# Performance work log

Hardware: AMD Instinct MI355X
Metric: run time of the kernel (lower is better)

The kernel has to match this reference:

```python
import jax, jax.numpy as jnp
import numpy as np

EPS = 1e-5
C = 1.0
SQRT_C = 1.0
MAX_NORM = 0.95


def _log0(y):
    # log map at origin: atanh(sqrt(c)||y||) * y / (sqrt(c)||y||)
    norm = jnp.clip(jnp.linalg.norm(y, axis=-1, keepdims=True), EPS)
    arg = jnp.clip(SQRT_C * norm, None, 1.0 - EPS)
    return jnp.arctanh(arg) * y / (SQRT_C * norm)


def _exp0(v):
    # exp map at origin: tanh(sqrt(c)||v||) * v / (sqrt(c)||v||)
    norm = jnp.clip(jnp.linalg.norm(v, axis=-1, keepdims=True), EPS)
    return jnp.tanh(SQRT_C * norm) * v / (SQRT_C * norm)


def _proj(x):
    # project onto Poincare ball of radius MAX_NORM/sqrt(c)
    max_r = MAX_NORM / SQRT_C
    norm = jnp.linalg.norm(x, axis=-1, keepdims=True)
    return jnp.where(norm > max_r, x * max_r / jnp.clip(norm, EPS), x)


def _hyp_linear(x, W, b):
    # log -> euclidean linear -> exp -> project
    v = _log0(x)
    v = v @ W.T + b
    return _proj(_exp0(v))


def _hyp_graph_conv(x, src, dst, n_nodes, Wm, bm, Wu, bu):
    # 1. hyperbolic linear message transform
    h = _hyp_linear(x, Wm, bm)
    # 2. tangent-space (hyperbolic) mean aggregation over incoming edges
    t = _log0(h[src])                                   # [E, D]
    summed = jax.ops.segment_sum(t, dst, num_segments=n_nodes)
    cnt = jax.ops.segment_sum(jnp.ones((src.shape[0], 1), t.dtype), dst,
                              num_segments=n_nodes)
    agg = _proj(_exp0(summed / jnp.clip(cnt, 1.0)))
    # 3. hyperbolic linear update
    return _hyp_linear(agg, Wu, bu)


def setup_inputs() -> dict:
    key = jax.random.key(0)
    k1, k2, k3, k4 = jax.random.split(key, 4)
    N, E, D, L = 50000, 800000, 128, 2
    x = jax.random.normal(k1, (N, D), dtype=jnp.float32) * 0.01
    edge_index = jax.random.randint(k2, (2, E), 0, N, dtype=jnp.int32)
    msg_W = jax.random.normal(k3, (L, D, D), dtype=jnp.float32) * 0.05
    msg_b = jnp.zeros((L, D), dtype=jnp.float32)
    upd_W = jax.random.normal(k4, (L, D, D), dtype=jnp.float32) * 0.05
    upd_b = jnp.zeros((L, D), dtype=jnp.float32)
    return {"x": x, "edge_index": edge_index, "msg_W": msg_W, "msg_b": msg_b,
            "upd_W": upd_W, "upd_b": upd_b}


def reference(x, edge_index, msg_W, msg_b, upd_W, upd_b):
    src, dst = edge_index[0], edge_index[1]
    n_nodes = x.shape[0]
    h = x
    for l in range(msg_W.shape[0]):  # small fixed layer count
        h = _hyp_graph_conv(h, src, dst, n_nodes,
                            msg_W[l], msg_b[l], upd_W[l], upd_b[l])
    return h
```

## Files before the change

### kernel.cpp

```cpp
#include <hip/hip_runtime.h>
#include <math.h>

#define EPSF 1e-5f
#define MAXN 0.95f
#define DD 128

typedef unsigned short u16;
typedef __attribute__((ext_vector_type(8))) __bf16 bf16x8;
typedef __attribute__((ext_vector_type(4))) float f32x4;
typedef __attribute__((ext_vector_type(8))) unsigned short u16x8;
typedef __attribute__((ext_vector_type(4))) unsigned u32x4;

#define MFMA16 __builtin_amdgcn_mfma_f32_16x16x32_bf16

__device__ __forceinline__ u16 f2bf(float f) {
    unsigned u = __float_as_uint(f);
    return (u16)((u + 0x7FFFu + ((u >> 16) & 1u)) >> 16);
}
__device__ __forceinline__ float bf2f(u16 b) {
    return __uint_as_float(((unsigned)b) << 16);
}

__device__ __forceinline__ float chain_scale(float nrm, bool log_out) {
    float nc  = fmaxf(nrm, EPSF);
    float f   = tanhf(nc) / nc;
    float wn  = f * nrm;
    float p   = (wn > MAXN) ? (MAXN / fmaxf(wn, EPSF)) : 1.f;
    float s   = f * p;
    if (log_out) {
        float n2  = wn * p;
        float n2c = fmaxf(n2, EPSF);
        float arg = fminf(n2c, 1.f - EPSF);
        s *= atanhf(arg) / n2c;
    }
    return s;
}

__device__ __forceinline__ float agg_scale(const float* __restrict__ ssum,
                                           const int* __restrict__ rowptr,
                                           int rg) {
    int cnt = max(rowptr[rg + 1] - rowptr[rg], 1);
    float inv = 1.f / (float)cnt;
    return chain_scale(sqrtf(ssum[rg]) * inv, true) * inv;
}

__global__ __launch_bounds__(256)
void zero_int4(int4* __restrict__ p, int n4)
{
    int i = blockIdx.x * 256 + threadIdx.x;
    if (i < n4) p[i] = make_int4(0, 0, 0, 0);
}

__global__ __launch_bounds__(256)
void split_w(const float* __restrict__ msgW, const float* __restrict__ updW,
             u16* __restrict__ whi, u16* __restrict__ wlo, int L)
{
    int gid = blockIdx.x * 256 + threadIdx.x;
    int total = L * 2 * DD * DD;
    if (gid >= total) return;
    int mat = gid >> 14;
    int elem = gid & (DD * DD - 1);
    int l = mat >> 1, tpe = mat & 1;
    float f = (tpe ? updW : msgW)[(size_t)l * DD * DD + elem];
    u16 hb = f2bf(f);
    whi[gid] = hb;
    wlo[gid] = f2bf(f - bf2f(hb));
}

template<int LOG_OUT, int FP32_OUT, int F32_IN, int SCALE_IN>
__global__ __launch_bounds__(256)
void mfma_linear(const u16* __restrict__ vhi, const float* __restrict__ xin,
                 const float* __restrict__ ssum, const int* __restrict__ rowptr,
                 const u16* __restrict__ whi, const u16* __restrict__ wlo,
                 const float* __restrict__ bias,
                 u16* __restrict__ ohi, float* __restrict__ ofp, int N)
{
    __shared__ float sred[4][32];
    __shared__ float sScale[32];
    __shared__ float sSin[SCALE_IN ? 32 : 1];
    __shared__ u16 sHi[FP32_OUT ? 1 : 32][136];

    const int tid  = threadIdx.x;
    const int w    = tid >> 6;
    const int lane = tid & 63;
    const int l15  = lane & 15, lk = lane >> 4;
    const int base = blockIdx.x * 32;

    if (SCALE_IN) {
        if (tid < 32) {
            int rg = base + tid;
            sSin[tid] = agg_scale(ssum, rowptr, rg < N ? rg : (N - 1));
        }
        __syncthreads();
    }

    bf16x8 wh[2][4], wl[2][4];
    #pragma unroll
    for (int nt = 0; nt < 2; ++nt) {
        const int j = w * 32 + nt * 16 + l15;
        #pragma unroll
        for (int kt = 0; kt < 4; ++kt) {
            const int off = j * DD + kt * 32 + lk * 8;
            wh[nt][kt] = *(const bf16x8*)(whi + off);
            wl[nt][kt] = *(const bf16x8*)(wlo + off);
        }
    }
    const float bv0 = bias[w * 32 + l15];
    const float bv1 = bias[w * 32 + 16 + l15];

    f32x4 acc[2][2];
    #pragma unroll
    for (int mt = 0; mt < 2; ++mt)
        #pragma unroll
        for (int nt = 0; nt < 2; ++nt)
            acc[mt][nt] = (f32x4){0.f, 0.f, 0.f, 0.f};

    #pragma unroll
    for (int mt = 0; mt < 2; ++mt) {
        int row = base + mt * 16 + l15;
        row = (row < N) ? row : (N - 1);
        bf16x8 ah[4];
        if (F32_IN) {
            const float* xr = xin + (size_t)row * DD + lk * 8;
            float fv[32];
            float ss = 0.f;
            #pragma unroll
            for (int kt = 0; kt < 4; ++kt) {
                float4 a = *(const float4*)(xr + kt * 32);
                float4 b = *(const float4*)(xr + kt * 32 + 4);
                fv[kt*8+0]=a.x; fv[kt*8+1]=a.y; fv[kt*8+2]=a.z; fv[kt*8+3]=a.w;
                fv[kt*8+4]=b.x; fv[kt*8+5]=b.y; fv[kt*8+6]=b.z; fv[kt*8+7]=b.w;
            }
            #pragma unroll
            for (int q = 0; q < 32; ++q) ss += fv[q] * fv[q];
            ss += __shfl_xor(ss, 16);
            ss += __shfl_xor(ss, 32);
            float nc = fmaxf(sqrtf(ss), EPSF);
            float sc = atanhf(fminf(nc, 1.f - EPSF)) / nc;
            #pragma unroll
            for (int kt = 0; kt < 4; ++kt) {
                u16x8 uh;
                #pragma unroll
                for (int q = 0; q < 8; ++q)
                    uh[q] = f2bf(fv[kt*8+q] * sc);
                ah[kt] = *reinterpret_cast<bf16x8*>(&uh);
            }
        } else {
            const size_t ro = (size_t)row * DD + lk * 8;
            #pragma unroll
            for (int kt = 0; kt < 4; ++kt)
                ah[kt] = *(const bf16x8*)(vhi + ro + kt * 32);
        }
        #pragma unroll
        for (int kt = 0; kt < 4; ++kt) {
            #pragma unroll
            for (int nt = 0; nt < 2; ++nt) {
                acc[mt][nt] = MFMA16(ah[kt], wh[nt][kt], acc[mt][nt], 0, 0, 0);
                acc[mt][nt] = MFMA16(ah[kt], wl[nt][kt], acc[mt][nt], 0, 0, 0);
            }
        }
    }

    #pragma unroll
    for (int mt = 0; mt < 2; ++mt) {
        #pragma unroll
        for (int r = 0; r < 4; ++r) {
            const float sv = SCALE_IN ? sSin[mt*16 + lk*4 + r] : 1.f;
            float y0 = acc[mt][0][r] * sv + bv0;
            float y1 = acc[mt][1][r] * sv + bv1;
            float part = y0 * y0 + y1 * y1;
            part += __shfl_xor(part, 1);
            part += __shfl_xor(part, 2);
            part += __shfl_xor(part, 4);
            part += __shfl_xor(part, 8);
            if (l15 == 0) sred[w][mt*16 + lk*4 + r] = part;
        }
    }
    __syncthreads();
    if (tid < 32) {
        float ss = sred[0][tid] + sred[1][tid] + sred[2][tid] + sred[3][tid];
        sScale[tid] = chain_scale(sqrtf(ss), LOG_OUT != 0);
    }
    __syncthreads();

    #pragma unroll
    for (int mt = 0; mt < 2; ++mt) {
        #pragma unroll
        for (int r = 0; r < 4; ++r) {
            const int rloc = mt*16 + lk*4 + r;
            const float s = sScale[rloc];
            const float sv = SCALE_IN ? sSin[rloc] : 1.f;
            #pragma unroll
            for (int nt = 0; nt < 2; ++nt) {
                float z = (acc[mt][nt][r] * sv + (nt ? bv1 : bv0)) * s;
                const int col = w*32 + nt*16 + l15;
                if (FP32_OUT) {
                    const int rg = base + rloc;
                    if (rg < N) ofp[(size_t)rg * DD + col] = z;
                } else {
                    sHi[rloc][col] = f2bf(z);
                }
            }
        }
    }
    if (!FP32_OUT) {
        __syncthreads();
        const int row = tid >> 3, qc = (tid & 7) * 16;
        const int rg = base + row;
        if (rg < N) {
            #pragma unroll
            for (int i = 0; i < 2; ++i)
                *(u16x8*)(ohi + (size_t)rg * DD + qc + i*8) =
                    *(const u16x8*)(&sHi[row][qc + i*8]);
        }
    }
}

__global__ __launch_bounds__(256)
void mfma_linear_fused(const u16* __restrict__ vhi,
                       const float* __restrict__ ssum, const int* __restrict__ rowptr,
                       const u16* __restrict__ wuh, const u16* __restrict__ wul,
                       const float* __restrict__ bu,
                       const u16* __restrict__ wmh, const u16* __restrict__ wml,
                       const float* __restrict__ bm,
                       u16* __restrict__ ohi, int N)
{
    __shared__ float sred[4][32];
    __shared__ float sScale[32];
    __shared__ float sSin[32];
    __shared__ u16 sHi[32][136];

    const int tid  = threadIdx.x;
    const int w    = tid >> 6;
    const int lane = tid & 63;
    const int l15  = lane & 15, lk = lane >> 4;
    const int base = blockIdx.x * 32;

    if (tid < 32) {
        int rg = base + tid;
        sSin[tid] = agg_scale(ssum, rowptr, rg < N ? rg : (N - 1));
    }
    __syncthreads();

    f32x4 acc[2][2];

    {
        bf16x8 wh[2][4], wl[2][4];
        #pragma unroll
        for (int nt = 0; nt < 2; ++nt) {
            const int j = w * 32 + nt * 16 + l15;
            #pragma unroll
            for (int kt = 0; kt < 4; ++kt) {
                const int off = j * DD + kt * 32 + lk * 8;
                wh[nt][kt] = *(const bf16x8*)(wuh + off);
                wl[nt][kt] = *(const bf16x8*)(wul + off);
            }
        }
        const float bv0 = bu[w * 32 + l15];
        const float bv1 = bu[w * 32 + 16 + l15];

        #pragma unroll
        for (int mt = 0; mt < 2; ++mt)
            #pragma unroll
            for (int nt = 0; nt < 2; ++nt)
                acc[mt][nt] = (f32x4){0.f, 0.f, 0.f, 0.f};

        #pragma unroll
        for (int mt = 0; mt < 2; ++mt) {
            int row = base + mt * 16 + l15;
            row = (row < N) ? row : (N - 1);
            const size_t ro = (size_t)row * DD + lk * 8;
            bf16x8 ah[4];
            #pragma unroll
            for (int kt = 0; kt < 4; ++kt)
                ah[kt] = *(const bf16x8*)(vhi + ro + kt * 32);
            #pragma unroll
            for (int kt = 0; kt < 4; ++kt) {
                #pragma unroll
                for (int nt = 0; nt < 2; ++nt) {
                    acc[mt][nt] = MFMA16(ah[kt], wh[nt][kt], acc[mt][nt], 0, 0, 0);
                    acc[mt][nt] = MFMA16(ah[kt], wl[nt][kt], acc[mt][nt], 0, 0, 0);
                }
            }
        }

        #pragma unroll
        for (int mt = 0; mt < 2; ++mt) {
            #pragma unroll
            for (int r = 0; r < 4; ++r) {
                const float sv = sSin[mt*16 + lk*4 + r];
                float y0 = acc[mt][0][r] * sv + bv0;
                float y1 = acc[mt][1][r] * sv + bv1;
                float part = y0 * y0 + y1 * y1;
                part += __shfl_xor(part, 1);
                part += __shfl_xor(part, 2);
                part += __shfl_xor(part, 4);
                part += __shfl_xor(part, 8);
                if (l15 == 0) sred[w][mt*16 + lk*4 + r] = part;
            }
        }
        __syncthreads();
        if (tid < 32) {
            float ss = sred[0][tid] + sred[1][tid] + sred[2][tid] + sred[3][tid];
            sScale[tid] = chain_scale(sqrtf(ss), true);
        }
        __syncthreads();
        #pragma unroll
        for (int mt = 0; mt < 2; ++mt) {
            #pragma unroll
            for (int r = 0; r < 4; ++r) {
                const int rloc = mt*16 + lk*4 + r;
                const float s = sScale[rloc];
                const float sv = sSin[rloc];
                #pragma unroll
                for (int nt = 0; nt < 2; ++nt) {
                    float z = (acc[mt][nt][r] * sv + (nt ? bv1 : bv0)) * s;
                    sHi[rloc][w*32 + nt*16 + l15] = f2bf(z);
                }
            }
        }
    }
    __syncthreads();

    {
        bf16x8 wh[2][4], wl[2][4];
        #pragma unroll
        for (int nt = 0; nt < 2; ++nt) {
            const int j = w * 32 + nt * 16 + l15;
            #pragma unroll
            for (int kt = 0; kt < 4; ++kt) {
                const int off = j * DD + kt * 32 + lk * 8;
                wh[nt][kt] = *(const bf16x8*)(wmh + off);
                wl[nt][kt] = *(const bf16x8*)(wml + off);
            }
        }
        const float bv0 = bm[w * 32 + l15];
        const float bv1 = bm[w * 32 + 16 + l15];

        #pragma unroll
        for (int mt = 0; mt < 2; ++mt)
            #pragma unroll
            for (int nt = 0; nt < 2; ++nt)
                acc[mt][nt] = (f32x4){0.f, 0.f, 0.f, 0.f};

        #pragma unroll
        for (int mt = 0; mt < 2; ++mt) {
            const int r16 = mt * 16 + l15;
            bf16x8 ah[4];
            #pragma unroll
            for (int kt = 0; kt < 4; ++kt)
                ah[kt] = *(const bf16x8*)(&sHi[r16][kt * 32 + lk * 8]);
            #pragma unroll
            for (int kt = 0; kt < 4; ++kt) {
                #pragma unroll
                for (int nt = 0; nt < 2; ++nt) {
                    acc[mt][nt] = MFMA16(ah[kt], wh[nt][kt], acc[mt][nt], 0, 0, 0);
                    acc[mt][nt] = MFMA16(ah[kt], wl[nt][kt], acc[mt][nt], 0, 0, 0);
                }
            }
        }

        #pragma unroll
        for (int mt = 0; mt < 2; ++mt) {
            #pragma unroll
            for (int r = 0; r < 4; ++r) {
                float y0 = acc[mt][0][r] + bv0;
                float y1 = acc[mt][1][r] + bv1;
                float part = y0 * y0 + y1 * y1;
                part += __shfl_xor(part, 1);
                part += __shfl_xor(part, 2);
                part += __shfl_xor(part, 4);
                part += __shfl_xor(part, 8);
                if (l15 == 0) sred[w][mt*16 + lk*4 + r] = part;
            }
        }
        __syncthreads();
        if (tid < 32) {
            float ss = sred[0][tid] + sred[1][tid] + sred[2][tid] + sred[3][tid];
            sScale[tid] = chain_scale(sqrtf(ss), true);
        }
        __syncthreads();
        #pragma unroll
        for (int mt = 0; mt < 2; ++mt) {
            #pragma unroll
            for (int r = 0; r < 4; ++r) {
                const int rloc = mt*16 + lk*4 + r;
                const float s = sScale[rloc];
                #pragma unroll
                for (int nt = 0; nt < 2; ++nt) {
                    float z = (acc[mt][nt][r] + (nt ? bv1 : bv0)) * s;
                    sHi[rloc][w*32 + nt*16 + l15] = f2bf(z);
                }
            }
        }
        __syncthreads();
        const int row = tid >> 3, qc = (tid & 7) * 16;
        const int rg = base + row;
        if (rg < N) {
            #pragma unroll
            for (int i = 0; i < 2; ++i)
                *(u16x8*)(ohi + (size_t)rg * DD + qc + i*8) =
                    *(const u16x8*)(&sHi[row][qc + i*8]);
        }
    }
}

__global__ __launch_bounds__(256)
void degree_rank4(const int* __restrict__ dst, int* __restrict__ cnt4,
                  int* __restrict__ rank, int E, int N)
{
    int e4 = (blockIdx.x * 256 + threadIdx.x) * 4;
    if (e4 + 3 < E) {
        int4 d = *(const int4*)(dst + e4);
        int4 r;
        r.x = atomicAdd(&cnt4[0 * N + d.x], 1);
        r.y = atomicAdd(&cnt4[1 * N + d.y], 1);
        r.z = atomicAdd(&cnt4[2 * N + d.z], 1);
        r.w = atomicAdd(&cnt4[3 * N + d.w], 1);
        *(int4*)(rank + e4) = r;
    } else {
        for (int e = e4; e < E; ++e)
            rank[e] = atomicAdd(&cnt4[(e & 3) * N + dst[e]], 1);
    }
}

__global__ __launch_bounds__(256)
void combine_deg(const int* __restrict__ cnt4, int* __restrict__ deg, int N)
{
    int n = blockIdx.x * 256 + threadIdx.x;
    if (n >= N) return;
    deg[n] = cnt4[n] + cnt4[N + n] + cnt4[2 * N + n] + cnt4[3 * N + n];
}

__global__ __launch_bounds__(256)
void rpb_build(const int* __restrict__ cnt4, const int* __restrict__ rowptr,
               int* __restrict__ rpb, int N)
{
    int n = blockIdx.x * 256 + threadIdx.x;
    if (n >= N) return;
    int rp = rowptr[n];
    int c0 = cnt4[n], c1 = cnt4[N + n], c2 = cnt4[2 * N + n];
    rpb[n]         = rp;
    rpb[N + n]     = rp + c0;
    rpb[2 * N + n] = rp + c0 + c1;
    rpb[3 * N + n] = rp + c0 + c1 + c2;
}

__global__ __launch_bounds__(256)
void fill_csr4(const int* __restrict__ src, const int* __restrict__ dst,
               const int* __restrict__ rpb, const int* __restrict__ rank,
               int* __restrict__ csr, int E, int N)
{
    int e4 = (blockIdx.x * 256 + threadIdx.x) * 4;
    if (e4 + 3 < E) {
        int4 d = *(const int4*)(dst + e4);
        int4 r = *(const int4*)(rank + e4);
        int4 s = *(const int4*)(src + e4);
        csr[rpb[0 * N + d.x] + r.x] = s.x;
        csr[rpb[1 * N + d.y] + r.y] = s.y;
        csr[rpb[2 * N + d.z] + r.z] = s.z;
        csr[rpb[3 * N + d.w] + r.w] = s.w;
    } else {
        for (int e = e4; e < E; ++e)
            csr[rpb[(e & 3) * N + dst[e]] + rank[e]] = src[e];
    }
}

__global__ __launch_bounds__(1024)
void scan_rowptr(const int* __restrict__ deg, int* __restrict__ rowptr, int N)
{
    __shared__ int wsum[16];
    const int t = threadIdx.x, wv = t >> 6, ln = t & 63;
    int carry = 0;
    const int nch = (N + 4095) / 4096;
    for (int c = 0; c < nch; ++c) {
        const int i = c * 4096 + t * 4;
        int4 d = *(const int4*)(deg + i);
        int e1 = d.x, e2 = e1 + d.y, e3 = e2 + d.z, tot = e3 + d.w;
        int sc = tot;
        #pragma unroll
        for (int off = 1; off < 64; off <<= 1) {
            int u = __shfl_up(sc, off);
            if (ln >= off) sc += u;
        }
        if (ln == 63) wsum[wv] = sc;
        __syncthreads();
        if (wv == 0 && ln < 16) {
            int s2 = wsum[ln];
            #pragma unroll
            for (int off = 1; off < 16; off <<= 1) {
                int u = __shfl_up(s2, off);
                if (ln >= off) s2 += u;
            }
            wsum[ln] = s2;
        }
        __syncthreads();
        const int off0 = carry + ((wv > 0) ? wsum[wv - 1] : 0) + (sc - tot);
        if (i + 3 < N) {
            *(int4*)(rowptr + i) = make_int4(off0, off0 + e1, off0 + e2, off0 + e3);
        } else {
            if (i     < N) rowptr[i]     = off0;
            if (i + 1 < N) rowptr[i + 1] = off0 + e1;
            if (i + 2 < N) rowptr[i + 2] = off0 + e2;
        }
        carry += wsum[15];
        __syncthreads();
    }
    if (t == 0) rowptr[N] = carry;
}

__global__ __launch_bounds__(256)
void csr_gather_sum(const u16* __restrict__ ghi, const int* __restrict__ rowptr,
                    const int* __restrict__ csr, u16* __restrict__ ohi,
                    float* __restrict__ ssum, int N)
{
    int node = blockIdx.x * 4 + (threadIdx.x >> 6);
    if (node >= N) return;
    const int lane = threadIdx.x & 63;
    const int eg = lane >> 4, l15 = lane & 15;
    const int beg = rowptr[node], end = rowptr[node + 1];

    float acc[8] = {0.f,0.f,0.f,0.f,0.f,0.f,0.f,0.f};
    for (int b = beg; b < end; b += 64) {
        const int cnt = min(end - b, 64);
        const int myidx = (lane < cnt) ? csr[b + lane] : 0;
        u32x4 vc;
        {
            const bool act = eg < cnt;
            const int s = __shfl(myidx, act ? eg : 0);
            if (act) vc = *(const u32x4*)(ghi + (size_t)s * DD + l15 * 8);
        }
        for (int j = 0; j < cnt; j += 4) {
            const int en = j + 4 + eg;
            const bool actn = en < cnt;
            const int sn = __shfl(myidx, actn ? en : 0);
            u32x4 vn;
            if (actn) vn = *(const u32x4*)(ghi + (size_t)sn * DD + l15 * 8);
            if (j + eg < cnt) {
                #pragma unroll
                for (int p = 0; p < 4; ++p) {
                    acc[2*p+0] += __uint_as_float(vc[p] << 16);
                    acc[2*p+1] += __uint_as_float(vc[p] & 0xffff0000u);
                }
            }
            vc = vn;
        }
    }
    #pragma unroll
    for (int q = 0; q < 8; ++q) {
        acc[q] += __shfl_xor(acc[q], 16);
        acc[q] += __shfl_xor(acc[q], 32);
    }
    float ss = 0.f;
    #pragma unroll
    for (int q = 0; q < 8; ++q) ss += acc[q] * acc[q];
    ss += __shfl_xor(ss, 1); ss += __shfl_xor(ss, 2);
    ss += __shfl_xor(ss, 4); ss += __shfl_xor(ss, 8);
    if (eg == 0) {
        u32x4 hw;
        #pragma unroll
        for (int p = 0; p < 4; ++p) {
            u16 h0 = f2bf(acc[2*p+0]), h1 = f2bf(acc[2*p+1]);
            hw[p] = (unsigned)h0 | ((unsigned)h1 << 16);
        }
        *(u32x4*)(ohi + (size_t)node * DD + l15 * 8) = hw;
        if (l15 == 0) ssum[node] = ss;
    }
}

extern "C" void kernel_launch(void* const* d_in, const int* in_sizes, int n_in,
                              void* d_out, int out_size, void* d_ws, size_t ws_size,
                              hipStream_t stream)
{
    const float* x     = (const float*)d_in[0];
    const int*   ei    = (const int*)d_in[1];
    const float* msg_W = (const float*)d_in[2];
    const float* msg_b = (const float*)d_in[3];
    const float* upd_W = (const float*)d_in[4];
    const float* upd_b = (const float*)d_in[5];

    const int N = in_sizes[0] / DD;
    const int E = in_sizes[1] / 2;
    const int L = in_sizes[2] / (DD * DD);

    const int* src = ei;
    const int* dst = ei + E;

    u16* Ahi  = (u16*)d_ws;
    u16* WhiA = Ahi + (size_t)N * DD;
    u16* WloA = WhiA + (size_t)2 * L * DD * DD;
    int* deg  = (int*)(WloA + (size_t)2 * L * DD * DD);
    const int degCap = ((N + 4095) / 4096) * 4096;
    int* rowptr = deg + degCap;
    int* csr    = rowptr + (N + 1);
    float* ssum = (float*)(csr + E);
    int* cnt4   = (int*)(ssum + N);
    int* rpb    = cnt4 + 4 * (size_t)N;

    u16* Bhi  = (u16*)d_out;
    int* rank = (int*)(Bhi + (size_t)N * DD);

    const int nodeBlocks  = (N + 31) / 32;
    const int aggBlocks   = (N + 3) / 4;
    const int edge4Blocks = ((E + 3) / 4 + 255) / 256;
    const int nodeThreads = (N + 255) / 256;

    zero_int4<<<((4 * N) / 4 + 255) / 256, 256, 0, stream>>>((int4*)cnt4, (4 * N) / 4);
    {
        const int padStart4 = (N & ~3) / 4;
        zero_int4<<<(degCap / 4 - padStart4 + 255) / 256, 256, 0, stream>>>(
            (int4*)deg + padStart4, degCap / 4 - padStart4);
    }
    degree_rank4<<<edge4Blocks, 256, 0, stream>>>(dst, cnt4, rank, E, N);
    combine_deg<<<nodeThreads, 256, 0, stream>>>(cnt4, deg, N);
    scan_rowptr<<<1, 1024, 0, stream>>>(deg, rowptr, N);
    rpb_build<<<nodeThreads, 256, 0, stream>>>(cnt4, rowptr, rpb, N);
    fill_csr4<<<edge4Blocks, 256, 0, stream>>>(src, dst, rpb, rank, csr, E, N);
    split_w<<<(2 * L * DD * DD + 255) / 256, 256, 0, stream>>>(
        msg_W, upd_W, WhiA, WloA, L);

    mfma_linear<1, 0, 1, 0><<<nodeBlocks, 256, 0, stream>>>(
        nullptr, x, nullptr, nullptr,
        WhiA, WloA, msg_b, Bhi, nullptr, N);

    for (int l = 0; l < L; ++l) {
        const u16* wuh = WhiA + (size_t)(l * 2 + 1) * DD * DD;
        const u16* wul = WloA + (size_t)(l * 2 + 1) * DD * DD;

        csr_gather_sum<<<aggBlocks, 256, 0, stream>>>(
            Bhi, rowptr, csr, Ahi, ssum, N);

        if (l < L - 1) {
            const u16* wmh = WhiA + (size_t)((l + 1) * 2 + 0) * DD * DD;
            const u16* wml = WloA + (size_t)((l + 1) * 2 + 0) * DD * DD;
            mfma_linear_fused<<<nodeBlocks, 256, 0, stream>>>(
                Ahi, ssum, rowptr,
                wuh, wul, upd_b + (size_t)l * DD,
                wmh, wml, msg_b + (size_t)(l + 1) * DD,
                Bhi, N);
        } else {
            mfma_linear<0, 1, 0, 1><<<nodeBlocks, 256, 0, stream>>>(
                Ahi, nullptr, ssum, rowptr,
                wuh, wul, upd_b + (size_t)l * DD,
                nullptr, (float*)d_out, N);
        }
    }
}
```

Before: 241.6 us.

## Fuse CSR gather-sum aggregation into the following MFMA linear kernel

The separate gather-sum kernel is removed. Each 32-node block now gathers its neighbour sums directly into shared memory, with each of the four waves handling 8 nodes in turn, then runs the update (and next message) linear on that tile. This drops the intermediate bf16 aggregate and ssum round-trips through global memory and saves one launch per layer, and ping-pong buffers replace the in-place output. In exchange, only 4 waves per block do the gather, so latency hiding for the irregular loads may drop compared with the previous one-node-per-wave grid of 4-node blocks.

Result: slower. 247.6 us (+2.5%).

```diff
diff --git a/kernel.cpp b/kernel.cpp
--- a/kernel.cpp
+++ b/kernel.cpp
@@ -36,14 +36,6 @@
     return s;
 }
 
-__device__ __forceinline__ float agg_scale(const float* __restrict__ ssum,
-                                           const int* __restrict__ rowptr,
-                                           int rg) {
-    int cnt = max(rowptr[rg + 1] - rowptr[rg], 1);
-    float inv = 1.f / (float)cnt;
-    return chain_scale(sqrtf(ssum[rg]) * inv, true) * inv;
-}
-
 __global__ __launch_bounds__(256)
 void zero_int4(int4* __restrict__ p, int n4)
 {
@@ -67,18 +59,15 @@
     wlo[gid] = f2bf(f - bf2f(hb));
 }
 
-template<int LOG_OUT, int FP32_OUT, int F32_IN, int SCALE_IN>
-__global__ __launch_bounds__(256)
-void mfma_linear(const u16* __restrict__ vhi, const float* __restrict__ xin,
-                 const float* __restrict__ ssum, const int* __restrict__ rowptr,
-                 const u16* __restrict__ whi, const u16* __restrict__ wlo,
-                 const float* __restrict__ bias,
-                 u16* __restrict__ ohi, float* __restrict__ ofp, int N)
+__global__ __launch_bounds__(256)
+void mfma_linear_x(const float* __restrict__ xin,
+                   const u16* __restrict__ whi, const u16* __restrict__ wlo,
+                   const float* __restrict__ bias,
+                   u16* __restrict__ ohi, int N)
 {
     __shared__ float sred[4][32];
     __shared__ float sScale[32];
-    __shared__ float sSin[SCALE_IN ? 32 : 1];
-    __shared__ u16 sHi[FP32_OUT ? 1 : 32][136];
+    __shared__ u16 sHi[32][136];
 
     const int tid  = threadIdx.x;
     const int w    = tid >> 6;
@@ -86,14 +75,6 @@
     const int l15  = lane & 15, lk = lane >> 4;
     const int base = blockIdx.x * 32;
 
-    if (SCALE_IN) {
-        if (tid < 32) {
-            int rg = base + tid;
-            sSin[tid] = agg_scale(ssum, rowptr, rg < N ? rg : (N - 1));
-        }
-        __syncthreads();
-    }
-
     bf16x8 wh[2][4], wl[2][4];
     #pragma unroll
     for (int nt = 0; nt < 2; ++nt) {
@@ -119,37 +100,30 @@
     for (int mt = 0; mt < 2; ++mt) {
         int row = base + mt * 16 + l15;
         row = (row < N) ? row : (N - 1);
+        const float* xr = xin + (size_t)row * DD + lk * 8;
+        float fv[32];
+        float ss = 0.f;
+        #pragma unroll
+        for (int kt = 0; kt < 4; ++kt) {
+            float4 a = *(const float4*)(xr + kt * 32);
+            float4 b = *(const float4*)(xr + kt * 32 + 4);
+            fv[kt*8+0]=a.x; fv[kt*8+1]=a.y; fv[kt*8+2]=a.z; fv[kt*8+3]=a.w;
+            fv[kt*8+4]=b.x; fv[kt*8+5]=b.y; fv[kt*8+6]=b.z; fv[kt*8+7]=b.w;
+        }
+        #pragma unroll
+        for (int q = 0; q < 32; ++q) ss += fv[q] * fv[q];
+        ss += __shfl_xor(ss, 16);
+        ss += __shfl_xor(ss, 32);
+        float nc = fmaxf(sqrtf(ss), EPSF);
+        float sc = atanhf(fminf(nc, 1.f - EPSF)) / nc;
         bf16x8 ah[4];
-        if (F32_IN) {
-            const float* xr = xin + (size_t)row * DD + lk * 8;
-            float fv[32];
-            float ss = 0.f;
-            #pragma unroll
-            for (int kt = 0; kt < 4; ++kt) {
-                float4 a = *(const float4*)(xr + kt * 32);
-                float4 b = *(const float4*)(xr + kt * 32 + 4);
-                fv[kt*8+0]=a.x; fv[kt*8+1]=a.y; fv[kt*8+2]=a.z; fv[kt*8+3]=a.w;
-                fv[kt*8+4]=b.x; fv[kt*8+5]=b.y; fv[kt*8+6]=b.z; fv[kt*8+7]=b.w;
-            }
-            #pragma unroll
-            for (int q = 0; q < 32; ++q) ss += fv[q] * fv[q];
-            ss += __shfl_xor(ss, 16);
-            ss += __shfl_xor(ss, 32);
-            float nc = fmaxf(sqrtf(ss), EPSF);
-            float sc = atanhf(fminf(nc, 1.f - EPSF)) / nc;
-            #pragma unroll
-            for (int kt = 0; kt < 4; ++kt) {
-                u16x8 uh;
-                #pragma unroll
-                for (int q = 0; q < 8; ++q)
-                    uh[q] = f2bf(fv[kt*8+q] * sc);
-                ah[kt] = *reinterpret_cast<bf16x8*>(&uh);
-            }
-        } else {
-            const size_t ro = (size_t)row * DD + lk * 8;
-            #pragma unroll
-            for (int kt = 0; kt < 4; ++kt)
-                ah[kt] = *(const bf16x8*)(vhi + ro + kt * 32);
+        #pragma unroll
+        for (int kt = 0; kt < 4; ++kt) {
+            u16x8 uh;
+            #pragma unroll
+            for (int q = 0; q < 8; ++q)
+                uh[q] = f2bf(fv[kt*8+q] * sc);
+            ah[kt] = *reinterpret_cast<bf16x8*>(&uh);
         }
         #pragma unroll
         for (int kt = 0; kt < 4; ++kt) {
@@ -165,7 +139,180 @@
     for (int mt = 0; mt < 2; ++mt) {
         #pragma unroll
         for (int r = 0; r < 4; ++r) {
-            const float sv = SCALE_IN ? sSin[mt*16 + lk*4 + r] : 1.f;
+            float y0 = acc[mt][0][r] + bv0;
+            float y1 = acc[mt][1][r] + bv1;
+            float part = y0 * y0 + y1 * y1;
+            part += __shfl_xor(part, 1);
+            part += __shfl_xor(part, 2);
+            part += __shfl_xor(part, 4);
+            part += __shfl_xor(part, 8);
+            if (l15 == 0) sred[w][mt*16 + lk*4 + r] = part;
+        }
+    }
+    __syncthreads();
+    if (tid < 32) {
+        float ss = sred[0][tid] + sred[1][tid] + sred[2][tid] + sred[3][tid];
+        sScale[tid] = chain_scale(sqrtf(ss), true);
+    }
+    __syncthreads();
+
+    #pragma unroll
+    for (int mt = 0; mt < 2; ++mt) {
+        #pragma unroll
+        for (int r = 0; r < 4; ++r) {
+            const int rloc = mt*16 + lk*4 + r;
+            const float s = sScale[rloc];
+            #pragma unroll
+            for (int nt = 0; nt < 2; ++nt) {
+                float z = (acc[mt][nt][r] + (nt ? bv1 : bv0)) * s;
+                sHi[rloc][w*32 + nt*16 + l15] = f2bf(z);
+            }
+        }
+    }
+    __syncthreads();
+    const int row = tid >> 3, qc = (tid & 7) * 16;
+    const int rg = base + row;
+    if (rg < N) {
+        #pragma unroll
+        for (int i = 0; i < 2; ++i)
+            *(u16x8*)(ohi + (size_t)rg * DD + qc + i*8) =
+                *(const u16x8*)(&sHi[row][qc + i*8]);
+    }
+}
+
+__device__ __forceinline__ void gather_node(const u16* __restrict__ ghi,
+                                            const int* __restrict__ csr,
+                                            int beg, int end, int lane,
+                                            int eg, int l15, float acc[8])
+{
+    for (int b = beg; b < end; b += 64) {
+        const int cnt = min(end - b, 64);
+        const int myidx = (lane < cnt) ? csr[b + lane] : 0;
+        u32x4 vc;
+        {
+            const bool act = eg < cnt;
+            const int s = __shfl(myidx, act ? eg : 0);
+            if (act) vc = *(const u32x4*)(ghi + (size_t)s * DD + l15 * 8);
+        }
+        for (int j = 0; j < cnt; j += 4) {
+            const int en = j + 4 + eg;
+            const bool actn = en < cnt;
+            const int sn = __shfl(myidx, actn ? en : 0);
+            u32x4 vn;
+            if (actn) vn = *(const u32x4*)(ghi + (size_t)sn * DD + l15 * 8);
+            if (j + eg < cnt) {
+                #pragma unroll
+                for (int p = 0; p < 4; ++p) {
+                    acc[2*p+0] += __uint_as_float(vc[p] << 16);
+                    acc[2*p+1] += __uint_as_float(vc[p] & 0xffff0000u);
+                }
+            }
+            vc = vn;
+        }
+    }
+}
+
+template<int FINAL>
+__global__ __launch_bounds__(256)
+void gather_linear(const u16* __restrict__ ghi,
+                   const int* __restrict__ rowptr, const int* __restrict__ csr,
+                   const u16* __restrict__ w1h, const u16* __restrict__ w1l,
+                   const float* __restrict__ b1,
+                   const u16* __restrict__ w2h, const u16* __restrict__ w2l,
+                   const float* __restrict__ b2,
+                   u16* __restrict__ ohi, float* __restrict__ ofp, int N)
+{
+    __shared__ u16 sA[32][136];
+    __shared__ float sSin[32];
+    __shared__ float sred[4][32];
+    __shared__ float sScale[32];
+
+    const int tid  = threadIdx.x;
+    const int w    = tid >> 6;
+    const int lane = tid & 63;
+    const int l15  = lane & 15, lk = lane >> 4;
+    const int eg   = lane >> 4;
+    const int base = blockIdx.x * 32;
+
+    #pragma unroll 1
+    for (int i = 0; i < 8; ++i) {
+        const int node = base + w * 8 + i;
+        const int nc   = (node < N) ? node : (N - 1);
+        const int beg  = rowptr[nc], end = rowptr[nc + 1];
+        float acc[8] = {0.f,0.f,0.f,0.f,0.f,0.f,0.f,0.f};
+        gather_node(ghi, csr, beg, end, lane, eg, l15, acc);
+        #pragma unroll
+        for (int q = 0; q < 8; ++q) {
+            acc[q] += __shfl_xor(acc[q], 16);
+            acc[q] += __shfl_xor(acc[q], 32);
+        }
+        float ss = 0.f;
+        #pragma unroll
+        for (int q = 0; q < 8; ++q) ss += acc[q] * acc[q];
+        ss += __shfl_xor(ss, 1); ss += __shfl_xor(ss, 2);
+        ss += __shfl_xor(ss, 4); ss += __shfl_xor(ss, 8);
+        if (eg == 0) {
+            u32x4 hw;
+            #pragma unroll
+            for (int p = 0; p < 4; ++p) {
+                u16 h0 = f2bf(acc[2*p+0]), h1 = f2bf(acc[2*p+1]);
+                hw[p] = (unsigned)h0 | ((unsigned)h1 << 16);
+            }
+            *(u32x4*)(&sA[w*8 + i][l15 * 8]) = hw;
+        }
+        if (lane == 0) {
+            int cntv = max(end - beg, 1);
+            float inv = 1.f / (float)cntv;
+            sSin[w*8 + i] = chain_scale(sqrtf(ss) * inv, true) * inv;
+        }
+    }
+    __syncthreads();
+
+    f32x4 acc[2][2];
+    float bv0, bv1;
+    {
+        bf16x8 wh[2][4], wl[2][4];
+        #pragma unroll
+        for (int nt = 0; nt < 2; ++nt) {
+            const int j = w * 32 + nt * 16 + l15;
+            #pragma unroll
+            for (int kt = 0; kt < 4; ++kt) {
+                const int off = j * DD + kt * 32 + lk * 8;
+                wh[nt][kt] = *(const bf16x8*)(w1h + off);
+                wl[nt][kt] = *(const bf16x8*)(w1l + off);
+            }
+        }
+        bv0 = b1[w * 32 + l15];
+        bv1 = b1[w * 32 + 16 + l15];
+
+        #pragma unroll
+        for (int mt = 0; mt < 2; ++mt)
+            #pragma unroll
+            for (int nt = 0; nt < 2; ++nt)
+                acc[mt][nt] = (f32x4){0.f, 0.f, 0.f, 0.f};
+
+        #pragma unroll
+        for (int mt = 0; mt < 2; ++mt) {
+            bf16x8 ah[4];
+            #pragma unroll
+            for (int kt = 0; kt < 4; ++kt)
+                ah[kt] = *(const bf16x8*)(&sA[mt*16 + l15][kt * 32 + lk * 8]);
+            #pragma unroll
+            for (int kt = 0; kt < 4; ++kt) {
+                #pragma unroll
+                for (int nt = 0; nt < 2; ++nt) {
+                    acc[mt][nt] = MFMA16(ah[kt], wh[nt][kt], acc[mt][nt], 0, 0, 0);
+                    acc[mt][nt] = MFMA16(ah[kt], wl[nt][kt], acc[mt][nt], 0, 0, 0);
+                }
+            }
+        }
+    }
+
+    #pragma unroll
+    for (int mt = 0; mt < 2; ++mt) {
+        #pragma unroll
+        for (int r = 0; r < 4; ++r) {
+            const float sv = sSin[mt*16 + lk*4 + r];
             float y0 = acc[mt][0][r] * sv + bv0;
             float y1 = acc[mt][1][r] * sv + bv1;
             float part = y0 * y0 + y1 * y1;
@@ -179,9 +326,30 @@
     __syncthreads();
     if (tid < 32) {
         float ss = sred[0][tid] + sred[1][tid] + sred[2][tid] + sred[3][tid];
-        sScale[tid] = chain_scale(sqrtf(ss), LOG_OUT != 0);
-    }
-    __syncthreads();
+        sScale[tid] = chain_scale(sqrtf(ss), FINAL ? false : true);
+    }
+    __syncthreads();
+
+    if (FINAL) {
+        #pragma unroll
+        for (int mt = 0; mt < 2; ++mt) {
+            #pragma unroll
+            for (int r = 0; r < 4; ++r) {
+                const int rloc = mt*16 + lk*4 + r;
+                const float s = sScale[rloc];
+                const float sv = sSin[rloc];
+                const int rg = base + rloc;
+                if (rg < N) {
+                    #pragma unroll
+                    for (int nt = 0; nt < 2; ++nt) {
+                        float z = (acc[mt][nt][r] * sv + (nt ? bv1 : bv0)) * s;
+                        ofp[(size_t)rg * DD + w*32 + nt*16 + l15] = z;
+                    }
+                }
+            }
+        }
+        return;
+    }
 
     #pragma unroll
     for (int mt = 0; mt < 2; ++mt) {
@@ -189,60 +357,15 @@
         for (int r = 0; r < 4; ++r) {
             const int rloc = mt*16 + lk*4 + r;
             const float s = sScale[rloc];
-            const float sv = SCALE_IN ? sSin[rloc] : 1.f;
+            const float sv = sSin[rloc];
             #pragma unroll
             for (int nt = 0; nt < 2; ++nt) {
                 float z = (acc[mt][nt][r] * sv + (nt ? bv1 : bv0)) * s;
-                const int col = w*32 + nt*16 + l15;
-                if (FP32_OUT) {
-                    const int rg = base + rloc;
-                    if (rg < N) ofp[(size_t)rg * DD + col] = z;
-                } else {
-                    sHi[rloc][col] = f2bf(z);
-                }
-            }
-        }
-    }
-    if (!FP32_OUT) {
-        __syncthreads();
-        const int row = tid >> 3, qc = (tid & 7) * 16;
-        const int rg = base + row;
-        if (rg < N) {
-            #pragma unroll
-            for (int i = 0; i < 2; ++i)
-                *(u16x8*)(ohi + (size_t)rg * DD + qc + i*8) =
-                    *(const u16x8*)(&sHi[row][qc + i*8]);
-        }
-    }
-}
-
-__global__ __launch_bounds__(256)
-void mfma_linear_fused(const u16* __restrict__ vhi,
-                       const float* __restrict__ ssum, const int* __restrict__ rowptr,
-                       const u16* __restrict__ wuh, const u16* __restrict__ wul,
-                       const float* __restrict__ bu,
-                       const u16* __restrict__ wmh, const u16* __restrict__ wml,
-                       const float* __restrict__ bm,
-                       u16* __restrict__ ohi, int N)
-{
-    __shared__ float sred[4][32];
-    __shared__ float sScale[32];
-    __shared__ float sSin[32];
-    __shared__ u16 sHi[32][136];
-
-    const int tid  = threadIdx.x;
-    const int w    = tid >> 6;
-    const int lane = tid & 63;
-    const int l15  = lane & 15, lk = lane >> 4;
-    const int base = blockIdx.x * 32;
-
-    if (tid < 32) {
-        int rg = base + tid;
-        sSin[tid] = agg_scale(ssum, rowptr, rg < N ? rg : (N - 1));
-    }
-    __syncthreads();
-
-    f32x4 acc[2][2];
+                sA[rloc][w*32 + nt*16 + l15] = f2bf(z);
+            }
+        }
+    }
+    __syncthreads();
 
     {
         bf16x8 wh[2][4], wl[2][4];
@@ -252,12 +375,12 @@
             #pragma unroll
             for (int kt = 0; kt < 4; ++kt) {
                 const int off = j * DD + kt * 32 + lk * 8;
-                wh[nt][kt] = *(const bf16x8*)(wuh + off);
-                wl[nt][kt] = *(const bf16x8*)(wul + off);
-            }
-        }
-        const float bv0 = bu[w * 32 + l15];
-        const float bv1 = bu[w * 32 + 16 + l15];
+                wh[nt][kt] = *(const bf16x8*)(w2h + off);
+                wl[nt][kt] = *(const bf16x8*)(w2l + off);
+            }
+        }
+        bv0 = b2[w * 32 + l15];
+        bv1 = b2[w * 32 + 16 + l15];
 
         #pragma unroll
         for (int mt = 0; mt < 2; ++mt)
@@ -267,13 +390,10 @@
 
         #pragma unroll
         for (int mt = 0; mt < 2; ++mt) {
-            int row = base + mt * 16 + l15;
-            row = (row < N) ? row : (N - 1);
-            const size_t ro = (size_t)row * DD + lk * 8;
             bf16x8 ah[4];
             #pragma unroll
             for (int kt = 0; kt < 4; ++kt)
-                ah[kt] = *(const bf16x8*)(vhi + ro + kt * 32);
+                ah[kt] = *(const bf16x8*)(&sA[mt*16 + l15][kt * 32 + lk * 8]);
             #pragma unroll
             for (int kt = 0; kt < 4; ++kt) {
                 #pragma unroll
@@ -283,125 +403,49 @@
                 }
             }
         }
-
-        #pragma unroll
-        for (int mt = 0; mt < 2; ++mt) {
-            #pragma unroll
-            for (int r = 0; r < 4; ++r) {
-                const float sv = sSin[mt*16 + lk*4 + r];
-                float y0 = acc[mt][0][r] * sv + bv0;
-                float y1 = acc[mt][1][r] * sv + bv1;
-                float part = y0 * y0 + y1 * y1;
-                part += __shfl_xor(part, 1);
-                part += __shfl_xor(part, 2);
-                part += __shfl_xor(part, 4);
-                part += __shfl_xor(part, 8);
-                if (l15 == 0) sred[w][mt*16 + lk*4 + r] = part;
-            }
-        }
-        __syncthreads();
-        if (tid < 32) {
-            float ss = sred[0][tid] + sred[1][tid] + sred[2][tid] + sred[3][tid];
-            sScale[tid] = chain_scale(sqrtf(ss), true);
-        }
-        __syncthreads();
-        #pragma unroll
-        for (int mt = 0; mt < 2; ++mt) {
-            #pragma unroll
-            for (int r = 0; r < 4; ++r) {
-                const int rloc = mt*16 + lk*4 + r;
-                const float s = sScale[rloc];
-                const float sv = sSin[rloc];
-                #pragma unroll
-                for (int nt = 0; nt < 2; ++nt) {
-                    float z = (acc[mt][nt][r] * sv + (nt ? bv1 : bv0)) * s;
-                    sHi[rloc][w*32 + nt*16 + l15] = f2bf(z);
-                }
-            }
-        }
-    }
-    __syncthreads();
-
-    {
-        bf16x8 wh[2][4], wl[2][4];
-        #pragma unroll
-        for (int nt = 0; nt < 2; ++nt) {
-            const int j = w * 32 + nt * 16 + l15;
-            #pragma unroll
-            for (int kt = 0; kt < 4; ++kt) {
-                const int off = j * DD + kt * 32 + lk * 8;
-                wh[nt][kt] = *(const bf16x8*)(wmh + off);
-                wl[nt][kt] = *(const bf16x8*)(wml + off);
-            }
-        }
-        const float bv0 = bm[w * 32 + l15];
-        const float bv1 = bm[w * 32 + 16 + l15];
-
-        #pragma unroll
-        for (int mt = 0; mt < 2; ++mt)
-            #pragma unroll
-            for (int nt = 0; nt < 2; ++nt)
-                acc[mt][nt] = (f32x4){0.f, 0.f, 0.f, 0.f};
-
-        #pragma unroll
-        for (int mt = 0; mt < 2; ++mt) {
-            const int r16 = mt * 16 + l15;
-            bf16x8 ah[4];
-            #pragma unroll
-            for (int kt = 0; kt < 4; ++kt)
-                ah[kt] = *(const bf16x8*)(&sHi[r16][kt * 32 + lk * 8]);
-            #pragma unroll
-            for (int kt = 0; kt < 4; ++kt) {
-                #pragma unroll
-                for (int nt = 0; nt < 2; ++nt) {
-                    acc[mt][nt] = MFMA16(ah[kt], wh[nt][kt], acc[mt][nt], 0, 0, 0);
-                    acc[mt][nt] = MFMA16(ah[kt], wl[nt][kt], acc[mt][nt], 0, 0, 0);
-                }
-            }
-        }
-
-        #pragma unroll
-        for (int mt = 0; mt < 2; ++mt) {
-            #pragma unroll
-            for (int r = 0; r < 4; ++r) {
-                float y0 = acc[mt][0][r] + bv0;
-                float y1 = acc[mt][1][r] + bv1;
-                float part = y0 * y0 + y1 * y1;
-                part += __shfl_xor(part, 1);
-                part += __shfl_xor(part, 2);
-                part += __shfl_xor(part, 4);
-                part += __shfl_xor(part, 8);
-                if (l15 == 0) sred[w][mt*16 + lk*4 + r] = part;
-            }
-        }
-        __syncthreads();
-        if (tid < 32) {
-            float ss = sred[0][tid] + sred[1][tid] + sred[2][tid] + sred[3][tid];
-            sScale[tid] = chain_scale(sqrtf(ss), true);
-        }
-        __syncthreads();
-        #pragma unroll
-        for (int mt = 0; mt < 2; ++mt) {
-            #pragma unroll
-            for (int r = 0; r < 4; ++r) {
-                const int rloc = mt*16 + lk*4 + r;
-                const float s = sScale[rloc];
-                #pragma unroll
-                for (int nt = 0; nt < 2; ++nt) {
-                    float z = (acc[mt][nt][r] + (nt ? bv1 : bv0)) * s;
-                    sHi[rloc][w*32 + nt*16 + l15] = f2bf(z);
-                }
-            }
-        }
-        __syncthreads();
-        const int row = tid >> 3, qc = (tid & 7) * 16;
-        const int rg = base + row;
-        if (rg < N) {
-            #pragma unroll
-            for (int i = 0; i < 2; ++i)
-                *(u16x8*)(ohi + (size_t)rg * DD + qc + i*8) =
-                    *(const u16x8*)(&sHi[row][qc + i*8]);
-        }
+    }
+
+    #pragma unroll
+    for (int mt = 0; mt < 2; ++mt) {
+        #pragma unroll
+        for (int r = 0; r < 4; ++r) {
+            float y0 = acc[mt][0][r] + bv0;
+            float y1 = acc[mt][1][r] + bv1;
+            float part = y0 * y0 + y1 * y1;
+            part += __shfl_xor(part, 1);
+            part += __shfl_xor(part, 2);
+            part += __shfl_xor(part, 4);
+            part += __shfl_xor(part, 8);
+            if (l15 == 0) sred[w][mt*16 + lk*4 + r] = part;
+        }
+    }
+    __syncthreads();
+    if (tid < 32) {
+        float ss = sred[0][tid] + sred[1][tid] + sred[2][tid] + sred[3][tid];
+        sScale[tid] = chain_scale(sqrtf(ss), true);
+    }
+    __syncthreads();
+    #pragma unroll
+    for (int mt = 0; mt < 2; ++mt) {
+        #pragma unroll
+        for (int r = 0; r < 4; ++r) {
+            const int rloc = mt*16 + lk*4 + r;
+            const float s = sScale[rloc];
+            #pragma unroll
+            for (int nt = 0; nt < 2; ++nt) {
+                float z = (acc[mt][nt][r] + (nt ? bv1 : bv0)) * s;
+                sA[rloc][w*32 + nt*16 + l15] = f2bf(z);
+            }
+        }
+    }
+    __syncthreads();
+    const int row = tid >> 3, qc = (tid & 7) * 16;
+    const int rg = base + row;
+    if (rg < N) {
+        #pragma unroll
+        for (int i = 0; i < 2; ++i)
+            *(u16x8*)(ohi + (size_t)rg * DD + qc + i*8) =
+                *(const u16x8*)(&sA[row][qc + i*8]);
     }
 }
 
@@ -509,65 +553,6 @@
     if (t == 0) rowptr[N] = carry;
 }
 
-__global__ __launch_bounds__(256)
-void csr_gather_sum(const u16* __restrict__ ghi, const int* __restrict__ rowptr,
-                    const int* __restrict__ csr, u16* __restrict__ ohi,
-                    float* __restrict__ ssum, int N)
-{
-    int node = blockIdx.x * 4 + (threadIdx.x >> 6);
-    if (node >= N) return;
-    const int lane = threadIdx.x & 63;
-    const int eg = lane >> 4, l15 = lane & 15;
-    const int beg = rowptr[node], end = rowptr[node + 1];
-
-    float acc[8] = {0.f,0.f,0.f,0.f,0.f,0.f,0.f,0.f};
-    for (int b = beg; b < end; b += 64) {
-        const int cnt = min(end - b, 64);
-        const int myidx = (lane < cnt) ? csr[b + lane] : 0;
-        u32x4 vc;
-        {
-            const bool act = eg < cnt;
-            const int s = __shfl(myidx, act ? eg : 0);
-            if (act) vc = *(const u32x4*)(ghi + (size_t)s * DD + l15 * 8);
-        }
-        for (int j = 0; j < cnt; j += 4) {
-            const int en = j + 4 + eg;
-            const bool actn = en < cnt;
-            const int sn = __shfl(myidx, actn ? en : 0);
-            u32x4 vn;
-            if (actn) vn = *(const u32x4*)(ghi + (size_t)sn * DD + l15 * 8);
-            if (j + eg < cnt) {
-                #pragma unroll
-                for (int p = 0; p < 4; ++p) {
-                    acc[2*p+0] += __uint_as_float(vc[p] << 16);
-                    acc[2*p+1] += __uint_as_float(vc[p] & 0xffff0000u);
-                }
-            }
-            vc = vn;
-        }
-    }
-    #pragma unroll
-    for (int q = 0; q < 8; ++q) {
-        acc[q] += __shfl_xor(acc[q], 16);
-        acc[q] += __shfl_xor(acc[q], 32);
-    }
-    float ss = 0.f;
-    #pragma unroll
-    for (int q = 0; q < 8; ++q) ss += acc[q] * acc[q];
-    ss += __shfl_xor(ss, 1); ss += __shfl_xor(ss, 2);
-    ss += __shfl_xor(ss, 4); ss += __shfl_xor(ss, 8);
-    if (eg == 0) {
-        u32x4 hw;
-        #pragma unroll
-        for (int p = 0; p < 4; ++p) {
-            u16 h0 = f2bf(acc[2*p+0]), h1 = f2bf(acc[2*p+1]);
-            hw[p] = (unsigned)h0 | ((unsigned)h1 << 16);
-        }
-        *(u32x4*)(ohi + (size_t)node * DD + l15 * 8) = hw;
-        if (l15 == 0) ssum[node] = ss;
-    }
-}
-
 extern "C" void kernel_launch(void* const* d_in, const int* in_sizes, int n_in,
                               void* d_out, int out_size, void* d_ws, size_t ws_size,
                               hipStream_t stream)
@@ -593,15 +578,13 @@
     const int degCap = ((N + 4095) / 4096) * 4096;
     int* rowptr = deg + degCap;
     int* csr    = rowptr + (N + 1);
-    float* ssum = (float*)(csr + E);
-    int* cnt4   = (int*)(ssum + N);
+    int* cnt4   = csr + E;
     int* rpb    = cnt4 + 4 * (size_t)N;
 
     u16* Bhi  = (u16*)d_out;
     int* rank = (int*)(Bhi + (size_t)N * DD);
 
     const int nodeBlocks  = (N + 31) / 32;
-    const int aggBlocks   = (N + 3) / 4;
     const int edge4Blocks = ((E + 3) / 4 + 255) / 256;
     const int nodeThreads = (N + 255) / 256;
 
@@ -619,29 +602,30 @@
     split_w<<<(2 * L * DD * DD + 255) / 256, 256, 0, stream>>>(
         msg_W, upd_W, WhiA, WloA, L);
 
-    mfma_linear<1, 0, 1, 0><<<nodeBlocks, 256, 0, stream>>>(
-        nullptr, x, nullptr, nullptr,
-        WhiA, WloA, msg_b, Bhi, nullptr, N);
+    u16* bufs[2] = {Bhi, Ahi};
+    int cur = ((L - 1) % 2 == 1) ? 0 : 1;
+
+    mfma_linear_x<<<nodeBlocks, 256, 0, stream>>>(
+        x, WhiA, WloA, msg_b, bufs[cur], N);
 
     for (int l = 0; l < L; ++l) {
         const u16* wuh = WhiA + (size_t)(l * 2 + 1) * DD * DD;
         const u16* wul = WloA + (size_t)(l * 2 + 1) * DD * DD;
 
-        csr_gather_sum<<<aggBlocks, 256, 0, stream>>>(
-            Bhi, rowptr, csr, Ahi, ssum, N);
-
         if (l < L - 1) {
             const u16* wmh = WhiA + (size_t)((l + 1) * 2 + 0) * DD * DD;
             const u16* wml = WloA + (size_t)((l + 1) * 2 + 0) * DD * DD;
-            mfma_linear_fused<<<nodeBlocks, 256, 0, stream>>>(
-                Ahi, ssum, rowptr,
+            gather_linear<0><<<nodeBlocks, 256, 0, stream>>>(
+                bufs[cur], rowptr, csr,
                 wuh, wul, upd_b + (size_t)l * DD,
                 wmh, wml, msg_b + (size_t)(l + 1) * DD,
-                Bhi, N);
+                bufs[cur ^ 1], nullptr, N);
+            cur ^= 1;
         } else {
-            mfma_linear<0, 1, 0, 1><<<nodeBlocks, 256, 0, stream>>>(
-                Ahi, nullptr, ssum, rowptr,
+            gather_linear<1><<<nodeBlocks, 256, 0, stream>>>(
+                bufs[cur], rowptr, csr,
                 wuh, wul, upd_b + (size_t)l * DD,
+                nullptr, nullptr, nullptr,
                 nullptr, (float*)d_out, N);
         }
     }
```
